# Optimization experiments

Measured on AMD Instinct MI355X. Metric: run time of the kernel, lower is better.

The kernel has to match this reference:

```python
import jax, jax.numpy as jnp
import numpy as np

B, S, H = 8, 4096, 1024
N_SPANS = 100   # output_shape
MAX_LEN = 64    # max span length (begin capped at S - MAX_LEN)


def setup_inputs() -> dict:
    key = jax.random.key(0)
    k1, k2, k3 = jax.random.split(key, 3)
    context = jax.random.normal(k1, (B, S, H), dtype=jnp.float32)
    spans_begin = jax.random.randint(k2, (B, N_SPANS), 0, S - MAX_LEN, dtype=jnp.int32)
    # length 0 encodes the torch begin==end case (pool the single token at begin)
    spans_len = jax.random.randint(k3, (B, N_SPANS), 0, MAX_LEN, dtype=jnp.int32)
    return {"context": context, "spans_begin": spans_begin, "spans_len": spans_len}


def reference(context, spans_begin, spans_len):
    # context: [B, S, H]; spans_begin/spans_len: [B, N]
    b, s, h = context.shape
    eff_len = jnp.maximum(spans_len, 1)                      # begin==end -> take single token
    pos = jnp.arange(MAX_LEN, dtype=jnp.int32)               # [L]
    idx = jnp.clip(spans_begin[:, :, None] + pos, 0, s - 1)  # [B, N, L]
    gathered = context[jnp.arange(b)[:, None, None], idx]    # [B, N, L, H]
    valid = pos[None, None, :] < eff_len[:, :, None]         # [B, N, L]
    neg_inf = jnp.array(-jnp.inf, dtype=context.dtype)
    pooled = jnp.where(valid[..., None], gathered, neg_inf).max(axis=2)  # [B, N, H]
    return pooled
```

## Files before the change

kernel.cpp:

```cpp
#include <hip/hip_runtime.h>
#include <math.h>

constexpr int B = 8;
constexpr int S = 4096;
constexpr int H = 1024;
constexpr int N_SPANS = 100;
constexpr int MAX_LEN = 64;

__global__ __launch_bounds__(256)
void maxpool_spans_kernel(const float* __restrict__ ctx,
                          const int* __restrict__ spans_begin,
                          const int* __restrict__ spans_len,
                          float* __restrict__ out)
{
    const int span = blockIdx.x;
    const int b    = span / N_SPANS;

    int bg = spans_begin[span];
    if (bg < 0) bg = 0;
    if (bg > S - MAX_LEN) bg = S - MAX_LEN;

    int ln = spans_len[span];
    if (ln < 1) ln = 1;
    if (ln > MAX_LEN) ln = MAX_LEN;

    const float4* __restrict__ row =
        (const float4*)(ctx) + ((size_t)b * S + (size_t)bg) * (H / 4) + threadIdx.x;
    const int stride = H / 4;

    float4 acc;
    acc.x = -INFINITY; acc.y = -INFINITY; acc.z = -INFINITY; acc.w = -INFINITY;

    #pragma unroll 4
    for (int p = 0; p < ln; ++p) {
        float4 v = row[(size_t)p * stride];
        acc.x = fmaxf(acc.x, v.x);
        acc.y = fmaxf(acc.y, v.y);
        acc.z = fmaxf(acc.z, v.z);
        acc.w = fmaxf(acc.w, v.w);
    }

    float4* __restrict__ o = (float4*)(out) + (size_t)span * (H / 4) + threadIdx.x;
    *o = acc;
}

extern "C" void kernel_launch(void* const* d_in, const int* in_sizes, int n_in,
                              void* d_out, int out_size, void* d_ws, size_t ws_size,
                              hipStream_t stream)
{
    const float* ctx        = (const float*)d_in[0];
    const int*   spans_begin = (const int*)d_in[1];
    const int*   spans_len   = (const int*)d_in[2];
    float*       out         = (float*)d_out;

    dim3 grid(B * N_SPANS);
    dim3 block(256);
    maxpool_spans_kernel<<<grid, block, 0, stream>>>(ctx, spans_begin, spans_len, out);
}
```

Before: 188.0 us.

## Split span pooling across H quarters and waves with shared-memory max reduction

```diff
diff --git a/kernel.cpp b/kernel.cpp
--- a/kernel.cpp
+++ b/kernel.cpp
@@ -6,6 +6,8 @@
 constexpr int H = 1024;
 constexpr int N_SPANS = 100;
 constexpr int MAX_LEN = 64;
+constexpr int F4_PER_ROW = H / 4;
+constexpr int QUARTER_F4 = 64;
 
 __global__ __launch_bounds__(256)
 void maxpool_spans_kernel(const float* __restrict__ ctx,
@@ -13,8 +15,11 @@
                           const int* __restrict__ spans_len,
                           float* __restrict__ out)
 {
-    const int span = blockIdx.x;
-    const int b    = span / N_SPANS;
+    const int span    = blockIdx.x;
+    const int quarter = blockIdx.y;
+    const int b       = span / N_SPANS;
+    const int wave    = threadIdx.x >> 6;
+    const int lane    = threadIdx.x & 63;
 
     int bg = spans_begin[span];
     if (bg < 0) bg = 0;
@@ -24,36 +29,50 @@
     if (ln < 1) ln = 1;
     if (ln > MAX_LEN) ln = MAX_LEN;
 
-    const float4* __restrict__ row =
-        (const float4*)(ctx) + ((size_t)b * S + (size_t)bg) * (H / 4) + threadIdx.x;
-    const int stride = H / 4;
+    const int f4 = quarter * QUARTER_F4 + lane;
+    const float4* __restrict__ base =
+        (const float4*)(ctx) + ((size_t)b * S + (size_t)bg) * F4_PER_ROW + f4;
 
     float4 acc;
     acc.x = -INFINITY; acc.y = -INFINITY; acc.z = -INFINITY; acc.w = -INFINITY;
 
     #pragma unroll 4
-    for (int p = 0; p < ln; ++p) {
-        float4 v = row[(size_t)p * stride];
+    for (int p = wave; p < ln; p += 4) {
+        float4 v = base[(size_t)p * F4_PER_ROW];
         acc.x = fmaxf(acc.x, v.x);
         acc.y = fmaxf(acc.y, v.y);
         acc.z = fmaxf(acc.z, v.z);
         acc.w = fmaxf(acc.w, v.w);
     }
 
-    float4* __restrict__ o = (float4*)(out) + (size_t)span * (H / 4) + threadIdx.x;
-    *o = acc;
+    __shared__ float4 red[256];
+    red[threadIdx.x] = acc;
+    __syncthreads();
+
+    if (wave == 0) {
+        float4 a = red[lane];
+        float4 b1 = red[64 + lane];
+        float4 c = red[128 + lane];
+        float4 d = red[192 + lane];
+        a.x = fmaxf(fmaxf(a.x, b1.x), fmaxf(c.x, d.x));
+        a.y = fmaxf(fmaxf(a.y, b1.y), fmaxf(c.y, d.y));
+        a.z = fmaxf(fmaxf(a.z, b1.z), fmaxf(c.z, d.z));
+        a.w = fmaxf(fmaxf(a.w, b1.w), fmaxf(c.w, d.w));
+        float4* __restrict__ o = (float4*)(out) + (size_t)span * F4_PER_ROW + f4;
+        *o = a;
+    }
 }
 
 extern "C" void kernel_launch(void* const* d_in, const int* in_sizes, int n_in,
                               void* d_out, int out_size, void* d_ws, size_t ws_size,
                               hipStream_t stream)
 {
-    const float* ctx        = (const float*)d_in[0];
+    const float* ctx         = (const float*)d_in[0];
     const int*   spans_begin = (const int*)d_in[1];
     const int*   spans_len   = (const int*)d_in[2];
     float*       out         = (float*)d_out;
 
-    dim3 grid(B * N_SPANS);
+    dim3 grid(B * N_SPANS, 4);
     dim3 block(256);
     maxpool_spans_kernel<<<grid, block, 0, stream>>>(ctx, spans_begin, spans_len, out);
 }
```

New measurement: 183.8 us. 2.2% less time.
